# Performance work log

Hardware: AMD Instinct MI355X
Metric: run time of the kernel (lower is better)

Reference implementation:

```python
import jax, jax.numpy as jnp
import numpy as np
from jax import lax

INPUT_DIM = 256
OUTPUT_DIM = 128
HIDDEN_DIM = 512
BATCH = 32768
T0, T1 = 0.0, 1.0
N_STEPS = 40  # fixed-step RK4 stand-in for adaptive odeint


def setup_inputs() -> dict:
    key = jax.random.key(0)
    ks = jax.random.split(key, 10)
    s_in = 1.0 / np.sqrt(INPUT_DIM)
    s_h = 1.0 / np.sqrt(HIDDEN_DIM)
    return {
        "x": jax.random.normal(ks[0], (BATCH, INPUT_DIM), dtype=jnp.float32),
        # input_x: Linear(input_dim -> hidden_dim)
        "Wx": jax.random.uniform(ks[1], (HIDDEN_DIM, INPUT_DIM), jnp.float32, -s_in, s_in),
        "bx": jax.random.uniform(ks[2], (HIDDEN_DIM,), jnp.float32, -s_in, s_in),
        # LiquidODEFunc params: dh/dt = (-h + tanh(W h + U u + b)) / tau
        "W": jax.random.uniform(ks[3], (HIDDEN_DIM, HIDDEN_DIM), jnp.float32, -s_h, s_h),
        "U": jax.random.uniform(ks[4], (HIDDEN_DIM, HIDDEN_DIM), jnp.float32, -s_h, s_h),
        "b": jax.random.uniform(ks[5], (HIDDEN_DIM,), jnp.float32, -s_h, s_h),
        "tau": jnp.ones((HIDDEN_DIM,), dtype=jnp.float32)
             + 0.1 * jax.random.uniform(ks[6], (HIDDEN_DIM,), jnp.float32),
        # forward_head: Linear(hidden_dim -> output_dim)
        "Wf": jax.random.uniform(ks[7], (OUTPUT_DIM, HIDDEN_DIM), jnp.float32, -s_h, s_h),
        "bf": jax.random.uniform(ks[8], (OUTPUT_DIM,), jnp.float32, -s_h, s_h),
    }


def reference(x, Wx, bx, W, U, b, tau, Wf, bf):
    # x -> latent projection
    u = x @ Wx.T + bx                       # (B, H)
    # input drive U u + b is constant over the ODE solve; precompute once
    drive = u @ U.T + b                     # (B, H)
    dt = (T1 - T0) / N_STEPS

    def f(h):
        return (-h + jnp.tanh(h @ W.T + drive)) / tau

    def rk4_step(h, _):
        k1 = f(h)
        k2 = f(h + 0.5 * dt * k1)
        k3 = f(h + 0.5 * dt * k2)
        k4 = f(h + dt * k3)
        return h + (dt / 6.0) * (k1 + 2.0 * k2 + 2.0 * k3 + k4), None

    h_T, _ = lax.scan(rk4_step, u, None, length=N_STEPS)  # h0 = u_proj
    return h_T @ Wf.T + bf                   # (B, output_dim)
```

## Files before the change

### kernel.cpp

```cpp
#include <hip/hip_runtime.h>
#include <stdint.h>

#define IN_DIM 256
#define HID 512
#define OUT_DIM 128
#define BT 64
#define NSTEPS 40
#define TPB 1024

typedef float f32x4 __attribute__((ext_vector_type(4)));
typedef __bf16 bf16x8 __attribute__((ext_vector_type(8)));

#define TANH_SC 2.8853900817779268f

static __device__ __forceinline__ uint32_t cvtpk(float a, float b) {
  uint32_t r;
  asm("v_cvt_pk_bf16_f32 %0, %1, %2" : "=v"(r) : "v"(a), "v"(b));
  return r;
}
static __device__ __forceinline__ float bflo(uint32_t u) {
  union { uint32_t u; float f; } v; v.u = u << 16; return v.f;
}
static __device__ __forceinline__ float bfhi(uint32_t u) {
  union { uint32_t u; float f; } v; v.u = u & 0xFFFF0000u; return v.f;
}
static __device__ __forceinline__ uint32_t pkh(float a, float b) {
  const uint16_t lo = __builtin_bit_cast(uint16_t, (_Float16)a);
  const uint16_t hi = __builtin_bit_cast(uint16_t, (_Float16)b);
  return (uint32_t)lo | ((uint32_t)hi << 16);
}
static __device__ __forceinline__ float h2lo(uint32_t u) {
  return (float)__builtin_bit_cast(_Float16, (uint16_t)(u & 0xFFFFu));
}
static __device__ __forceinline__ float h2hi(uint32_t u) {
  return (float)__builtin_bit_cast(_Float16, (uint16_t)(u >> 16));
}
static __device__ __forceinline__ float tanh_fast(float x) {
  const float e = __builtin_amdgcn_exp2f(x);
  return __builtin_fmaf(-2.0f, __builtin_amdgcn_rcpf(e + 1.0f), 1.0f);
}

static __device__ __forceinline__ int lds_ea(int m, int n) {
  return m * 1024 + ((((n >> 3) ^ (m & 15)) << 4)) + ((n & 7) << 1);
}

template <int NKSEG>
static __device__ __forceinline__ void mm_sw(const __bf16* __restrict__ Ap,
                                             const char* lds, int B1,
                                             f32x4 acc[2][4]) {
#pragma unroll 2
  for (int ks = 0; ks < NKSEG; ++ks) {
    const int ba = (B1 ^ ((ks & 3) << 6)) + ((ks >> 2) << 8);
    const bf16x8 wf0 = *(const bf16x8*)(Ap + (size_t)ks * 512);
    const bf16x8 wf1 = *(const bf16x8*)(Ap + (size_t)(NKSEG + ks) * 512);
#pragma unroll
    for (int j = 0; j < 4; ++j) {
      const bf16x8 hf = *(const bf16x8*)(lds + ba + j * 16384);
      acc[0][j] = __builtin_amdgcn_mfma_f32_16x16x32_bf16(wf0, hf, acc[0][j],
                                                          0, 0, 0);
      acc[1][j] = __builtin_amdgcn_mfma_f32_16x16x32_bf16(wf1, hf, acc[1][j],
                                                          0, 0, 0);
    }
  }
}

__global__ __launch_bounds__(TPB, 4) void liq_main(
    const float* __restrict__ x, const float* __restrict__ bx,
    const float* __restrict__ bvec, const float* __restrict__ tau,
    const float* __restrict__ bfh, const __bf16* __restrict__ Wx_p,
    const __bf16* __restrict__ U_p, const __bf16* __restrict__ W_p,
    const __bf16* __restrict__ Wf_p, float* __restrict__ out) {
  __shared__ __align__(16) char abuf[BT * 1024];
  __shared__ __align__(8) uint2 drv[8 * TPB];
  const int tid = threadIdx.x;
  const int w = tid >> 6;
  const int lane = tid & 63;
  const int l15 = lane & 15;
  const int q = lane >> 4;
  const int row0 = blockIdx.x * BT;

  const int B1 =
      l15 * 1024 + ((q ^ (l15 & 3)) << 4) + (((l15 >> 2) & 3) << 6);
  const int chunk0 = ((q >> 1) ^ (l15 & 1)) | (((l15 >> 1) & 1) << 1) |
                     ((4 * w) ^ (l15 & 12));
  const int A0 = l15 * 1024 + ((q & 1) << 3) + (chunk0 << 4);

  {
    const float4* x4 = (const float4*)(x + (size_t)row0 * IN_DIM);
#pragma unroll
    for (int it = 0; it < (BT * IN_DIM / 4) / TPB; ++it) {
      const int id = tid + it * TPB;
      const float4 v = x4[id];
      const int m = id >> 6;
      const int c = (id & 63) << 2;
      uint2 pk;
      pk.x = cvtpk(v.x, v.y);
      pk.y = cvtpk(v.z, v.w);
      *(uint2*)(abuf + lds_ea(m, c)) = pk;
    }
  }

  uint32_t itp[4];
#pragma unroll
  for (int i = 0; i < 2; ++i) {
    const float4 tv = *(const float4*)(tau + 32 * w + 16 * i + 4 * q);
    itp[i * 2] = cvtpk(1.0f / tv.x, 1.0f / tv.y);
    itp[i * 2 + 1] = cvtpk(1.0f / tv.z, 1.0f / tv.w);
  }
  __syncthreads();

  f32x4 acc[2][4];
#pragma unroll
  for (int i = 0; i < 2; ++i) {
    const float4 b4 = *(const float4*)(bx + 32 * w + 16 * i + 4 * q);
#pragma unroll
    for (int j = 0; j < 4; ++j) acc[i][j] = (f32x4){b4.x, b4.y, b4.z, b4.w};
  }
  mm_sw<IN_DIM / 32>(Wx_p + (size_t)w * 8192 + lane * 8, abuf, B1, acc);

  uint32_t h16[16];
#pragma unroll
  for (int i = 0; i < 2; ++i)
#pragma unroll
    for (int j = 0; j < 4; ++j) {
      const int ti = i * 4 + j;
      h16[ti * 2] = pkh(acc[i][j][0], acc[i][j][1]);
      h16[ti * 2 + 1] = pkh(acc[i][j][2], acc[i][j][3]);
    }

  __syncthreads();
#pragma unroll
  for (int i = 0; i < 2; ++i)
#pragma unroll
    for (int j = 0; j < 4; ++j) {
      uint2 pk;
      pk.x = cvtpk(acc[i][j][0], acc[i][j][1]);
      pk.y = cvtpk(acc[i][j][2], acc[i][j][3]);
      *(uint2*)(abuf + ((A0 ^ (i << 5)) + j * 16384)) = pk;
    }
  __syncthreads();

#pragma unroll
  for (int i = 0; i < 2; ++i) {
    const float4 b4 = *(const float4*)(bvec + 32 * w + 16 * i + 4 * q);
#pragma unroll
    for (int j = 0; j < 4; ++j)
      acc[i][j] = (f32x4){b4.x * TANH_SC, b4.y * TANH_SC, b4.z * TANH_SC,
                          b4.w * TANH_SC};
  }
  mm_sw<HID / 32>(U_p + (size_t)w * 16384 + lane * 8, abuf, B1, acc);
#pragma unroll
  for (int i = 0; i < 2; ++i)
#pragma unroll
    for (int j = 0; j < 4; ++j) {
      const int ti = i * 4 + j;
      uint2 pk;
      pk.x = cvtpk(acc[i][j][0], acc[i][j][1]);
      pk.y = cvtpk(acc[i][j][2], acc[i][j][3]);
      drv[ti * TPB + tid] = pk;
    }

  const float dt = 1.0f / NSTEPS;
  const float hdt = 0.5f * dt;
  const float dt6 = dt / 6.0f;
  uint32_t Sp[16];
  const __bf16* Wp_base = W_p + (size_t)w * 16384 + lane * 8;

  for (int st = 0; st < NSTEPS; ++st) {
    for (int e = 0; e < 4; ++e) {
#pragma unroll
      for (int i = 0; i < 2; ++i)
#pragma unroll
        for (int j = 0; j < 4; ++j) {
          const int ti = i * 4 + j;
          const uint2 d = drv[ti * TPB + tid];
          acc[i][j] = (f32x4){bflo(d.x), bfhi(d.x), bflo(d.y), bfhi(d.y)};
        }
      mm_sw<HID / 32>(Wp_base, abuf, B1, acc);

      const float wk = (e == 1 || e == 2) ? 2.0f : 1.0f;
      const float cn = (e < 2) ? hdt : dt;
#pragma unroll
      for (int i = 0; i < 2; ++i)
#pragma unroll
        for (int j = 0; j < 4; ++j) {
          const int ti = i * 4 + j;
          const int sa = (A0 ^ (i << 5)) + j * 16384;
          const float hc0 = h2lo(h16[ti * 2]), hc1 = h2hi(h16[ti * 2]);
          const float hc2 = h2lo(h16[ti * 2 + 1]), hc3 = h2hi(h16[ti * 2 + 1]);
          float hin[4];
          if (e == 0) {
            hin[0] = hc0; hin[1] = hc1; hin[2] = hc2; hin[3] = hc3;
          } else {
            const uint2 hb = *(const uint2*)(abuf + sa);
            hin[0] = bflo(hb.x); hin[1] = bfhi(hb.x);
            hin[2] = bflo(hb.y); hin[3] = bfhi(hb.y);
          }
          float kk[4];
          kk[0] = (tanh_fast(acc[i][j][0]) - hin[0]) * bflo(itp[i * 2]);
          kk[1] = (tanh_fast(acc[i][j][1]) - hin[1]) * bfhi(itp[i * 2]);
          kk[2] = (tanh_fast(acc[i][j][2]) - hin[2]) * bflo(itp[i * 2 + 1]);
          kk[3] = (tanh_fast(acc[i][j][3]) - hin[3]) * bfhi(itp[i * 2 + 1]);
          float n0, n1, n2, n3;
          if (e == 0) {
            Sp[ti * 2] = cvtpk(kk[0], kk[1]);
            Sp[ti * 2 + 1] = cvtpk(kk[2], kk[3]);
            n0 = __builtin_fmaf(cn, kk[0], hc0);
            n1 = __builtin_fmaf(cn, kk[1], hc1);
            n2 = __builtin_fmaf(cn, kk[2], hc2);
            n3 = __builtin_fmaf(cn, kk[3], hc3);
          } else if (e < 3) {
            const float s0 = __builtin_fmaf(wk, kk[0], bflo(Sp[ti * 2]));
            const float s1 = __builtin_fmaf(wk, kk[1], bfhi(Sp[ti * 2]));
            const float s2 = __builtin_fmaf(wk, kk[2], bflo(Sp[ti * 2 + 1]));
            const float s3 = __builtin_fmaf(wk, kk[3], bfhi(Sp[ti * 2 + 1]));
            Sp[ti * 2] = cvtpk(s0, s1);
            Sp[ti * 2 + 1] = cvtpk(s2, s3);
            n0 = __builtin_fmaf(cn, kk[0], hc0);
            n1 = __builtin_fmaf(cn, kk[1], hc1);
            n2 = __builtin_fmaf(cn, kk[2], hc2);
            n3 = __builtin_fmaf(cn, kk[3], hc3);
          } else {
            n0 = __builtin_fmaf(dt6, bflo(Sp[ti * 2]) + kk[0], hc0);
            n1 = __builtin_fmaf(dt6, bfhi(Sp[ti * 2]) + kk[1], hc1);
            n2 = __builtin_fmaf(dt6, bflo(Sp[ti * 2 + 1]) + kk[2], hc2);
            n3 = __builtin_fmaf(dt6, bfhi(Sp[ti * 2 + 1]) + kk[3], hc3);
            h16[ti * 2] = pkh(n0, n1);
            h16[ti * 2 + 1] = pkh(n2, n3);
          }
          acc[i][j][0] = n0; acc[i][j][1] = n1;
          acc[i][j][2] = n2; acc[i][j][3] = n3;
        }
      __syncthreads();
#pragma unroll
      for (int i = 0; i < 2; ++i)
#pragma unroll
        for (int j = 0; j < 4; ++j) {
          uint2 pk;
          pk.x = cvtpk(acc[i][j][0], acc[i][j][1]);
          pk.y = cvtpk(acc[i][j][2], acc[i][j][3]);
          *(uint2*)(abuf + ((A0 ^ (i << 5)) + j * 16384)) = pk;
        }
      __syncthreads();
    }
  }

  {
    const int ct = w & 7;
    const int j0 = (w >> 3) * 2;
    const float4 b4 = *(const float4*)(bfh + 16 * ct + 4 * q);
    f32x4 a2[2];
#pragma unroll
    for (int jj = 0; jj < 2; ++jj) a2[jj] = (f32x4){b4.x, b4.y, b4.z, b4.w};
#pragma unroll 2
    for (int ks = 0; ks < HID / 32; ++ks) {
      const bf16x8 wf =
          *(const bf16x8*)(Wf_p + (size_t)(ct * 16 + ks) * 512 + lane * 8);
      const int ba = (B1 ^ ((ks & 3) << 6)) + ((ks >> 2) << 8);
#pragma unroll
      for (int jj = 0; jj < 2; ++jj) {
        const bf16x8 hf = *(const bf16x8*)(abuf + ba + (j0 + jj) * 16384);
        a2[jj] =
            __builtin_amdgcn_mfma_f32_16x16x32_bf16(wf, hf, a2[jj], 0, 0, 0);
      }
    }
#pragma unroll
    for (int jj = 0; jj < 2; ++jj) {
      float4 o;
      o.x = a2[jj][0]; o.y = a2[jj][1]; o.z = a2[jj][2]; o.w = a2[jj][3];
      *(float4*)(out + (size_t)(row0 + 16 * (j0 + jj) + l15) * OUT_DIM +
                 16 * ct + 4 * q) = o;
    }
  }
}

__global__ void pack_bfrag(const float* __restrict__ src, __bf16* __restrict__ dst,
                           int K, int kslog, int total, float scale) {
  const int i = blockIdx.x * blockDim.x + threadIdx.x;
  if (i >= total) return;
  const int j = i & 7;
  const int lane = (i >> 3) & 63;
  const int rem = i >> 9;
  const int ks = rem & ((1 << kslog) - 1);
  const int nt = rem >> kslog;
  const int n = (nt << 4) + (lane & 15);
  const int k = (ks << 5) + ((lane >> 4) << 3) + j;
  dst[i] = (__bf16)(src[n * K + k] * scale);
}

extern "C" void kernel_launch(void* const* d_in, const int* in_sizes, int n_in,
                              void* d_out, int out_size, void* d_ws, size_t ws_size,
                              hipStream_t stream) {
  const float* x = (const float*)d_in[0];
  const float* Wx = (const float*)d_in[1];
  const float* bx = (const float*)d_in[2];
  const float* W = (const float*)d_in[3];
  const float* U = (const float*)d_in[4];
  const float* b = (const float*)d_in[5];
  const float* tau = (const float*)d_in[6];
  const float* Wf = (const float*)d_in[7];
  const float* bf_ = (const float*)d_in[8];
  float* out = (float*)d_out;

  char* ws = (char*)d_ws;
  __bf16* W_p = (__bf16*)(ws + 0);
  __bf16* U_p = (__bf16*)(ws + (512 * 1024));
  __bf16* Wx_p = (__bf16*)(ws + (1024 * 1024));
  __bf16* Wf_p = (__bf16*)(ws + (1280 * 1024));

  pack_bfrag<<<(HID * HID) / 256, 256, 0, stream>>>(W, W_p, HID, 4, HID * HID,
                                                    TANH_SC);
  pack_bfrag<<<(HID * HID) / 256, 256, 0, stream>>>(U, U_p, HID, 4, HID * HID,
                                                    TANH_SC);
  pack_bfrag<<<(HID * IN_DIM) / 256, 256, 0, stream>>>(Wx, Wx_p, IN_DIM, 3,
                                                       HID * IN_DIM, 1.0f);
  pack_bfrag<<<(OUT_DIM * HID) / 256, 256, 0, stream>>>(Wf, Wf_p, HID, 4,
                                                        OUT_DIM * HID, 1.0f);

  liq_main<<<32768 / BT, TPB, 0, stream>>>(x, bx, b, tau, bf_, Wx_p, U_p, W_p,
                                           Wf_p, out);
}
```

Measured before the change: 3.291 ms.

## Shrink batch tile to 32 rows with 4 waves each owning 128 hidden columns

Reduces the per-block batch tile from 64 to 32 rows and the block from 16 waves to 4. Each wave now computes 8 hidden-column tiles by 2 row tiles instead of 2 by 4, so each LDS-read h fragment feeds 8 MFMAs while each weight fragment is reused only twice. This doubles the number of blocks and cuts LDS and barrier cost per block, but raises the register footprint per thread (acc, h16, Sp, itp all grow) and the global weight-fetch traffic per row.

```diff
diff --git a/kernel.cpp b/kernel.cpp
--- a/kernel.cpp
+++ b/kernel.cpp
@@ -4,9 +4,9 @@
 #define IN_DIM 256
 #define HID 512
 #define OUT_DIM 128
-#define BT 64
+#define BT 32
 #define NSTEPS 40
-#define TPB 1024
+#define TPB 256
 
 typedef float f32x4 __attribute__((ext_vector_type(4)));
 typedef __bf16 bf16x8 __attribute__((ext_vector_type(8)));
@@ -47,31 +47,37 @@
 template <int NKSEG>
 static __device__ __forceinline__ void mm_sw(const __bf16* __restrict__ Ap,
                                              const char* lds, int B1,
-                                             f32x4 acc[2][4]) {
+                                             f32x4 acc[8][2]) {
 #pragma unroll 2
   for (int ks = 0; ks < NKSEG; ++ks) {
     const int ba = (B1 ^ ((ks & 3) << 6)) + ((ks >> 2) << 8);
-    const bf16x8 wf0 = *(const bf16x8*)(Ap + (size_t)ks * 512);
-    const bf16x8 wf1 = *(const bf16x8*)(Ap + (size_t)(NKSEG + ks) * 512);
-#pragma unroll
-    for (int j = 0; j < 4; ++j) {
-      const bf16x8 hf = *(const bf16x8*)(lds + ba + j * 16384);
-      acc[0][j] = __builtin_amdgcn_mfma_f32_16x16x32_bf16(wf0, hf, acc[0][j],
-                                                          0, 0, 0);
-      acc[1][j] = __builtin_amdgcn_mfma_f32_16x16x32_bf16(wf1, hf, acc[1][j],
-                                                          0, 0, 0);
-    }
-  }
-}
-
-__global__ __launch_bounds__(TPB, 4) void liq_main(
+#pragma unroll
+    for (int h = 0; h < 2; ++h) {
+      bf16x8 wf[4];
+#pragma unroll
+      for (int ii = 0; ii < 4; ++ii)
+        wf[ii] =
+            *(const bf16x8*)(Ap + (size_t)((h * 4 + ii) * NKSEG + ks) * 512);
+#pragma unroll
+      for (int j = 0; j < 2; ++j) {
+        const bf16x8 hf = *(const bf16x8*)(lds + ba + j * 16384);
+#pragma unroll
+        for (int ii = 0; ii < 4; ++ii)
+          acc[h * 4 + ii][j] = __builtin_amdgcn_mfma_f32_16x16x32_bf16(
+              wf[ii], hf, acc[h * 4 + ii][j], 0, 0, 0);
+      }
+    }
+  }
+}
+
+__global__ __launch_bounds__(TPB, 2) void liq_main(
     const float* __restrict__ x, const float* __restrict__ bx,
     const float* __restrict__ bvec, const float* __restrict__ tau,
     const float* __restrict__ bfh, const __bf16* __restrict__ Wx_p,
     const __bf16* __restrict__ U_p, const __bf16* __restrict__ W_p,
     const __bf16* __restrict__ Wf_p, float* __restrict__ out) {
   __shared__ __align__(16) char abuf[BT * 1024];
-  __shared__ __align__(8) uint2 drv[8 * TPB];
+  __shared__ __align__(8) uint2 drv[16 * TPB];
   const int tid = threadIdx.x;
   const int w = tid >> 6;
   const int lane = tid & 63;
@@ -81,9 +87,8 @@
 
   const int B1 =
       l15 * 1024 + ((q ^ (l15 & 3)) << 4) + (((l15 >> 2) & 3) << 6);
-  const int chunk0 = ((q >> 1) ^ (l15 & 1)) | (((l15 >> 1) & 1) << 1) |
-                     ((4 * w) ^ (l15 & 12));
-  const int A0 = l15 * 1024 + ((q & 1) << 3) + (chunk0 << 4);
+  const int A0 =
+      l15 * 1024 + ((q & 1) << 3) + ((((16 * w) + (q >> 1)) ^ l15) << 4);
 
   {
     const float4* x4 = (const float4*)(x + (size_t)row0 * IN_DIM);
@@ -100,39 +105,39 @@
     }
   }
 
-  uint32_t itp[4];
-#pragma unroll
-  for (int i = 0; i < 2; ++i) {
-    const float4 tv = *(const float4*)(tau + 32 * w + 16 * i + 4 * q);
+  uint32_t itp[16];
+#pragma unroll
+  for (int i = 0; i < 8; ++i) {
+    const float4 tv = *(const float4*)(tau + 128 * w + 16 * i + 4 * q);
     itp[i * 2] = cvtpk(1.0f / tv.x, 1.0f / tv.y);
     itp[i * 2 + 1] = cvtpk(1.0f / tv.z, 1.0f / tv.w);
   }
   __syncthreads();
 
-  f32x4 acc[2][4];
-#pragma unroll
-  for (int i = 0; i < 2; ++i) {
-    const float4 b4 = *(const float4*)(bx + 32 * w + 16 * i + 4 * q);
-#pragma unroll
-    for (int j = 0; j < 4; ++j) acc[i][j] = (f32x4){b4.x, b4.y, b4.z, b4.w};
-  }
-  mm_sw<IN_DIM / 32>(Wx_p + (size_t)w * 8192 + lane * 8, abuf, B1, acc);
-
-  uint32_t h16[16];
-#pragma unroll
-  for (int i = 0; i < 2; ++i)
-#pragma unroll
-    for (int j = 0; j < 4; ++j) {
-      const int ti = i * 4 + j;
+  f32x4 acc[8][2];
+#pragma unroll
+  for (int i = 0; i < 8; ++i) {
+    const float4 b4 = *(const float4*)(bx + 128 * w + 16 * i + 4 * q);
+#pragma unroll
+    for (int j = 0; j < 2; ++j) acc[i][j] = (f32x4){b4.x, b4.y, b4.z, b4.w};
+  }
+  mm_sw<IN_DIM / 32>(Wx_p + (size_t)w * 32768 + lane * 8, abuf, B1, acc);
+
+  uint32_t h16[32];
+#pragma unroll
+  for (int i = 0; i < 8; ++i)
+#pragma unroll
+    for (int j = 0; j < 2; ++j) {
+      const int ti = i * 2 + j;
       h16[ti * 2] = pkh(acc[i][j][0], acc[i][j][1]);
       h16[ti * 2 + 1] = pkh(acc[i][j][2], acc[i][j][3]);
     }
 
   __syncthreads();
 #pragma unroll
-  for (int i = 0; i < 2; ++i)
-#pragma unroll
-    for (int j = 0; j < 4; ++j) {
+  for (int i = 0; i < 8; ++i)
+#pragma unroll
+    for (int j = 0; j < 2; ++j) {
       uint2 pk;
       pk.x = cvtpk(acc[i][j][0], acc[i][j][1]);
       pk.y = cvtpk(acc[i][j][2], acc[i][j][3]);
@@ -141,19 +146,19 @@
   __syncthreads();
 
 #pragma unroll
-  for (int i = 0; i < 2; ++i) {
-    const float4 b4 = *(const float4*)(bvec + 32 * w + 16 * i + 4 * q);
-#pragma unroll
-    for (int j = 0; j < 4; ++j)
+  for (int i = 0; i < 8; ++i) {
+    const float4 b4 = *(const float4*)(bvec + 128 * w + 16 * i + 4 * q);
+#pragma unroll
+    for (int j = 0; j < 2; ++j)
       acc[i][j] = (f32x4){b4.x * TANH_SC, b4.y * TANH_SC, b4.z * TANH_SC,
                           b4.w * TANH_SC};
   }
-  mm_sw<HID / 32>(U_p + (size_t)w * 16384 + lane * 8, abuf, B1, acc);
-#pragma unroll
-  for (int i = 0; i < 2; ++i)
-#pragma unroll
-    for (int j = 0; j < 4; ++j) {
-      const int ti = i * 4 + j;
+  mm_sw<HID / 32>(U_p + (size_t)w * 65536 + lane * 8, abuf, B1, acc);
+#pragma unroll
+  for (int i = 0; i < 8; ++i)
+#pragma unroll
+    for (int j = 0; j < 2; ++j) {
+      const int ti = i * 2 + j;
       uint2 pk;
       pk.x = cvtpk(acc[i][j][0], acc[i][j][1]);
       pk.y = cvtpk(acc[i][j][2], acc[i][j][3]);
@@ -163,16 +168,16 @@
   const float dt = 1.0f / NSTEPS;
   const float hdt = 0.5f * dt;
   const float dt6 = dt / 6.0f;
-  uint32_t Sp[16];
-  const __bf16* Wp_base = W_p + (size_t)w * 16384 + lane * 8;
+  uint32_t Sp[32];
+  const __bf16* Wp_base = W_p + (size_t)w * 65536 + lane * 8;
 
   for (int st = 0; st < NSTEPS; ++st) {
     for (int e = 0; e < 4; ++e) {
 #pragma unroll
-      for (int i = 0; i < 2; ++i)
-#pragma unroll
-        for (int j = 0; j < 4; ++j) {
-          const int ti = i * 4 + j;
+      for (int i = 0; i < 8; ++i)
+#pragma unroll
+        for (int j = 0; j < 2; ++j) {
+          const int ti = i * 2 + j;
           const uint2 d = drv[ti * TPB + tid];
           acc[i][j] = (f32x4){bflo(d.x), bfhi(d.x), bflo(d.y), bfhi(d.y)};
         }
@@ -181,10 +186,10 @@
       const float wk = (e == 1 || e == 2) ? 2.0f : 1.0f;
       const float cn = (e < 2) ? hdt : dt;
 #pragma unroll
-      for (int i = 0; i < 2; ++i)
-#pragma unroll
-        for (int j = 0; j < 4; ++j) {
-          const int ti = i * 4 + j;
+      for (int i = 0; i < 8; ++i)
+#pragma unroll
+        for (int j = 0; j < 2; ++j) {
+          const int ti = i * 2 + j;
           const int sa = (A0 ^ (i << 5)) + j * 16384;
           const float hc0 = h2lo(h16[ti * 2]), hc1 = h2hi(h16[ti * 2]);
           const float hc2 = h2lo(h16[ti * 2 + 1]), hc3 = h2hi(h16[ti * 2 + 1]);
@@ -233,9 +238,9 @@
         }
       __syncthreads();
 #pragma unroll
-      for (int i = 0; i < 2; ++i)
-#pragma unroll
-        for (int j = 0; j < 4; ++j) {
+      for (int i = 0; i < 8; ++i)
+#pragma unroll
+        for (int j = 0; j < 2; ++j) {
           uint2 pk;
           pk.x = cvtpk(acc[i][j][0], acc[i][j][1]);
           pk.y = cvtpk(acc[i][j][2], acc[i][j][3]);
@@ -246,30 +251,32 @@
   }
 
   {
-    const int ct = w & 7;
-    const int j0 = (w >> 3) * 2;
-    const float4 b4 = *(const float4*)(bfh + 16 * ct + 4 * q);
-    f32x4 a2[2];
-#pragma unroll
-    for (int jj = 0; jj < 2; ++jj) a2[jj] = (f32x4){b4.x, b4.y, b4.z, b4.w};
+#pragma unroll
+    for (int cs = 0; cs < 2; ++cs) {
+      const int ct = 2 * w + cs;
+      const float4 b4 = *(const float4*)(bfh + 16 * ct + 4 * q);
+      f32x4 a2[2];
+#pragma unroll
+      for (int j = 0; j < 2; ++j) a2[j] = (f32x4){b4.x, b4.y, b4.z, b4.w};
 #pragma unroll 2
-    for (int ks = 0; ks < HID / 32; ++ks) {
-      const bf16x8 wf =
-          *(const bf16x8*)(Wf_p + (size_t)(ct * 16 + ks) * 512 + lane * 8);
-      const int ba = (B1 ^ ((ks & 3) << 6)) + ((ks >> 2) << 8);
-#pragma unroll
-      for (int jj = 0; jj < 2; ++jj) {
-        const bf16x8 hf = *(const bf16x8*)(abuf + ba + (j0 + jj) * 16384);
-        a2[jj] =
-            __builtin_amdgcn_mfma_f32_16x16x32_bf16(wf, hf, a2[jj], 0, 0, 0);
+      for (int ks = 0; ks < HID / 32; ++ks) {
+        const bf16x8 wf =
+            *(const bf16x8*)(Wf_p + (size_t)(ct * 16 + ks) * 512 + lane * 8);
+        const int ba = (B1 ^ ((ks & 3) << 6)) + ((ks >> 2) << 8);
+#pragma unroll
+        for (int j = 0; j < 2; ++j) {
+          const bf16x8 hf = *(const bf16x8*)(abuf + ba + j * 16384);
+          a2[j] =
+              __builtin_amdgcn_mfma_f32_16x16x32_bf16(wf, hf, a2[j], 0, 0, 0);
+        }
       }
-    }
-#pragma unroll
-    for (int jj = 0; jj < 2; ++jj) {
-      float4 o;
-      o.x = a2[jj][0]; o.y = a2[jj][1]; o.z = a2[jj][2]; o.w = a2[jj][3];
-      *(float4*)(out + (size_t)(row0 + 16 * (j0 + jj) + l15) * OUT_DIM +
-                 16 * ct + 4 * q) = o;
+#pragma unroll
+      for (int j = 0; j < 2; ++j) {
+        float4 o;
+        o.x = a2[j][0]; o.y = a2[j][1]; o.z = a2[j][2]; o.w = a2[j][3];
+        *(float4*)(out + (size_t)(row0 + 16 * j + l15) * OUT_DIM + 16 * ct +
+                   4 * q) = o;
+      }
     }
   }
 }
```

Measured after the change: 8.746 ms. 166% more time.
